# Optimization experiments

Measured on AMD Instinct MI355X. Metric: run time of the kernel, lower is better.

The kernel has to match this reference:

```python
import jax, jax.numpy as jnp
import numpy as np

B = 8; H = 128; W = 128; C = 256
NH = 16; HD = 16          # head_dim hard-coded to 16 in source
WS = 8; SS = 4            # window size / shift size
HID = 1024                # mlp hidden = 4 * C
SCALE = HD ** (-0.5)


def _rel_pos_index(ws):
    # same construction as torch buffer relative_position_index
    coords = np.stack(np.meshgrid(np.arange(ws), np.arange(ws), indexing='ij')).reshape(2, -1)
    rel = (coords[:, :, None] - coords[:, None, :]).transpose(1, 2, 0).copy()
    rel[..., 0] += ws - 1
    rel[..., 1] += ws - 1
    rel[..., 0] *= 2 * ws - 1
    return rel.sum(-1)  # (N, N) ints


def _attn_mask(h, w, ws, ss):
    # shifted-window mask, matches calculate_mask()
    img = np.zeros((h, w))
    sl = (slice(0, -ws), slice(-ws, -ss), slice(-ss, None))
    c = 0
    for hs in sl:
        for wsl in sl:
            img[hs, wsl] = c
            c += 1
    mw = img.reshape(h // ws, ws, w // ws, ws).transpose(0, 2, 1, 3).reshape(-1, ws * ws)
    d = mw[:, None, :] - mw[:, :, None]  # (nW, N, N)
    return np.where(d == 0, 0.0, -100.0).astype(np.float32)


def _ln(x, g, b, eps=1e-5):
    m = x.mean(-1, keepdims=True)
    v = ((x - m) ** 2).mean(-1, keepdims=True)
    return (x - m) * jax.lax.rsqrt(v + eps) * g + b


def setup_inputs() -> dict:
    key = jax.random.key(0)
    ks = jax.random.split(key, 12)
    inner = NH * HD
    std = 0.02
    return {
        'x': jax.random.normal(ks[0], (B, H * W, C), jnp.float32),
        'ln1_g': jnp.ones((C,), jnp.float32),
        'ln1_b': jnp.zeros((C,), jnp.float32),
        'q_w': jax.random.normal(ks[1], (C, inner), jnp.float32) * std,
        'q_b': jnp.zeros((inner,), jnp.float32),
        'k_w': jax.random.normal(ks[2], (C, inner), jnp.float32) * std,
        'k_b': jnp.zeros((inner,), jnp.float32),
        'v_w': jax.random.normal(ks[3], (C, inner), jnp.float32) * std,
        'v_b': jnp.zeros((inner,), jnp.float32),
        'rpb': jax.random.normal(ks[4], ((2 * WS - 1) * (2 * WS - 1), NH), jnp.float32) * std,
        'proj_w': jax.random.normal(ks[5], (inner, C), jnp.float32) * std,
        'proj_b': jnp.zeros((C,), jnp.float32),
        'ln2_g': jnp.ones((C,), jnp.float32),
        'ln2_b': jnp.zeros((C,), jnp.float32),
        'fc1_w': jax.random.normal(ks[6], (C, HID), jnp.float32) * std,
        'fc1_b': jnp.zeros((HID,), jnp.float32),
        'fc2_w': jax.random.normal(ks[7], (HID, C), jnp.float32) * std,
        'fc2_b': jnp.zeros((C,), jnp.float32),
        'H_in': 128,
        'W_in': 128,
    }


def reference(x, ln1_g, ln1_b, q_w, q_b, k_w, k_b, v_w, v_b, rpb,
              proj_w, proj_b, ln2_g, ln2_b, fc1_w, fc1_b, fc2_w, fc2_b,
              H_in, W_in):
    N = WS * WS
    nW = (H // WS) * (W // WS)
    idx = _rel_pos_index(WS)                       # static int (N, N)
    mask = jnp.asarray(_attn_mask(H, W, WS, SS))   # (nW, N, N)

    shortcut = x
    h = _ln(x, ln1_g, ln1_b).reshape(B, H, W, C)
    h = jnp.roll(h, (-SS, -SS), axis=(1, 2))
    # window partition -> (B*nW, N, C)
    h = h.reshape(B, H // WS, WS, W // WS, WS, C).transpose(0, 1, 3, 2, 4, 5)
    h = h.reshape(B * nW, N, C)

    q = (h @ q_w + q_b).reshape(-1, N, NH, HD).transpose(0, 2, 1, 3) * SCALE
    k = (h @ k_w + k_b).reshape(-1, N, NH, HD).transpose(0, 2, 1, 3)
    v = (h @ v_w + v_b).reshape(-1, N, NH, HD).transpose(0, 2, 1, 3)

    attn = jnp.einsum('bhnd,bhmd->bhnm', q, k)     # (B*nW, NH, N, N)
    bias = rpb[idx.reshape(-1)].reshape(N, N, NH).transpose(2, 0, 1)
    attn = attn + bias[None]
    attn = attn.reshape(B, nW, NH, N, N) + mask[None, :, None]
    attn = jax.nn.softmax(attn.reshape(B * nW, NH, N, N), axis=-1)

    o = jnp.einsum('bhnm,bhmd->bhnd', attn, v)
    o = o.transpose(0, 2, 1, 3).reshape(B * nW, N, NH * HD)
    o = o @ proj_w + proj_b

    # window reverse + roll back
    o = o.reshape(B, H // WS, W // WS, WS, WS, C).transpose(0, 1, 3, 2, 4, 5)
    o = o.reshape(B, H, W, C)
    o = jnp.roll(o, (SS, SS), axis=(1, 2)).reshape(B, H * W, C)

    x = shortcut + o
    h2 = _ln(x, ln2_g, ln2_b)
    h2 = jax.nn.gelu(h2 @ fc1_w + fc1_b, approximate=False)
    return x + (h2 @ fc2_w + fc2_b)
```

## Files before the change

kernel.cpp:

```cpp
#include <hip/hip_runtime.h>
#include <hip/hip_bf16.h>
#include <stdint.h>


#define SLOT ((size_t)64 << 20)

typedef __attribute__((ext_vector_type(8))) short bf16x8;
typedef __attribute__((ext_vector_type(4))) float f32x4;

union FU { float f; unsigned u; };

__device__ inline float bflo(unsigned p) { FU x; x.u = p << 16; return x.f; }
__device__ inline float bfhi(unsigned p) { FU x; x.u = p & 0xffff0000u; return x.f; }
__device__ inline unsigned short f2bf(float f) {
  FU x; x.f = f;
  unsigned r = x.u + 0x7fff + ((x.u >> 16) & 1);
  return (unsigned short)(r >> 16);
}
__device__ inline unsigned packbf2(float a, float b) {
  FU x, y; x.f = a; y.f = b;
  unsigned ra = (x.u + 0x7fff + ((x.u >> 16) & 1)) >> 16;
  unsigned rb = (y.u + 0x7fff + ((y.u >> 16) & 1)) & 0xffff0000u;
  return ra | rb;
}

__device__ inline float fast_gelu(float v) {
  return v / (1.0f + __expf(-1.702f * v));
}

__device__ inline void gload16(const void* g, void* l) {
  __builtin_amdgcn_global_load_lds(
      (const __attribute__((address_space(1))) unsigned int*)g,
      (__attribute__((address_space(3))) unsigned int*)l, 16, 0, 0);
}


__global__ __launch_bounds__(256) void build_qkvw(
    const float* __restrict__ qw, const float* __restrict__ kw, const float* __restrict__ vw,
    const float* __restrict__ qb, const float* __restrict__ kb, const float* __restrict__ vb,
    unsigned short* __restrict__ wt, float* __restrict__ bias) {
  int i = blockIdx.x * 256 + threadIdx.x;
  if (i < 768 * 256) {
    int n = i >> 8, c = i & 255;
    const float* w = (n < 256) ? qw : (n < 512 ? kw : vw);
    const float sc = (n < 256) ? 0.25f : 1.0f;
    int nn = n & 255;
    wt[i] = f2bf(sc * w[c * 256 + nn]);
  }
  if (i < 768) {
    bias[i] = (i < 256) ? 0.25f * qb[i] : (i < 512 ? kb[i - 256] : vb[i - 512]);
  }
}

__global__ __launch_bounds__(256) void wconv_t(
    const float* __restrict__ src, unsigned short* __restrict__ dst, int R, int C) {
  int i = blockIdx.x * 256 + threadIdx.x;
  if (i >= R * C) return;
  int n = i / R, c = i - n * R;
  dst[i] = f2bf(src[(size_t)c * C + n]);
}

__global__ __launch_bounds__(256) void ln1_roll_win(
    const float* __restrict__ x, const float* __restrict__ g, const float* __restrict__ b,
    unsigned short* __restrict__ hwin) {
  const int tok = blockIdx.x * 4 + (threadIdx.x >> 6);
  const int l = threadIdx.x & 63;
  const int n = tok & 63, wi = (tok >> 6) & 255, bb = tok >> 14;
  const int wh = wi >> 4, ww = wi & 15, r = n >> 3, c = n & 7;
  const int hs = (wh * 8 + r + 4) & 127;
  const int wsx = (ww * 8 + c + 4) & 127;
  const float* xr = x + ((size_t)bb * 16384 + hs * 128 + wsx) * 256;
  float4 v = *(const float4*)(xr + l * 4);
  float s = v.x + v.y + v.z + v.w;
#pragma unroll
  for (int off = 32; off; off >>= 1) s += __shfl_xor(s, off);
  const float mean = s * (1.f / 256.f);
  const float d0 = v.x - mean, d1 = v.y - mean, d2 = v.z - mean, d3 = v.w - mean;
  float vv = d0 * d0 + d1 * d1 + d2 * d2 + d3 * d3;
#pragma unroll
  for (int off = 32; off; off >>= 1) vv += __shfl_xor(vv, off);
  const float rs = rsqrtf(vv * (1.f / 256.f) + 1e-5f);
  float4 gg = *(const float4*)(g + l * 4);
  float4 bv = *(const float4*)(b + l * 4);
  uint2 outv;
  outv.x = packbf2(d0 * rs * gg.x + bv.x, d1 * rs * gg.y + bv.y);
  outv.y = packbf2(d2 * rs * gg.z + bv.z, d3 * rs * gg.w + bv.w);
  *(uint2*)(hwin + (size_t)tok * 256 + l * 4) = outv;
}

template <int EPI, int K, int N, int NBX>
__global__ __launch_bounds__(256) void gemm128(
    const unsigned short* __restrict__ A, const unsigned short* __restrict__ Bt,
    const float* __restrict__ bias, unsigned short* __restrict__ Cb,
    float* __restrict__ Cf) {
  __shared__ __align__(16) unsigned short smem[2][2][128 * 64];
  const int nwg = gridDim.x;
  const int q = nwg >> 3;
  const int swz = (blockIdx.x & 7) * q + (blockIdx.x >> 3);
  const int m0 = (swz / NBX) * 128;
  const int n0 = (swz % NBX) * 128;

  const int t = threadIdx.x, w = t >> 6, l = t & 63;
  const int lg = l >> 4, lm = l & 15;
  const int wr = w >> 1, wc = w & 1;

  const int srow = w * 32 + (l >> 3);
  const int scol = ((l & 7) ^ (l >> 3)) * 8;
  const unsigned short* Ap = A + (size_t)(m0 + srow) * K + scol;
  const unsigned short* Bp = Bt + (size_t)(n0 + srow) * K + scol;

  const int cb = n0 + wc * 64 + lm;
  f32x4 acc[4][4];
#pragma unroll
  for (int n = 0; n < 4; ++n) {
    const float bv = bias[cb + n * 16];
#pragma unroll
    for (int m = 0; m < 4; ++m) acc[m][n] = (f32x4){bv, bv, bv, bv};
  }

  constexpr int NT = K >> 6;
  const int cx = lg ^ (lm & 7);

#pragma unroll
  for (int i = 0; i < 4; ++i) {
    gload16(Ap + (size_t)(i * 8) * K, &smem[0][0][(w * 32 + i * 8) * 64]);
    gload16(Bp + (size_t)(i * 8) * K, &smem[0][1][(w * 32 + i * 8) * 64]);
  }
  __syncthreads();

#pragma unroll
  for (int kt = 0; kt < NT; ++kt) {
    const int cur = kt & 1;
    if (kt + 1 < NT) {
      const int ko = (kt + 1) << 6;
#pragma unroll
      for (int i = 0; i < 4; ++i) {
        gload16(Ap + (size_t)(i * 8) * K + ko, &smem[cur ^ 1][0][(w * 32 + i * 8) * 64]);
        gload16(Bp + (size_t)(i * 8) * K + ko, &smem[cur ^ 1][1][(w * 32 + i * 8) * 64]);
      }
    }
#pragma unroll
    for (int kk = 0; kk < 64; kk += 32) {
      const int ch = (cx ^ (kk >> 3)) * 8;
      bf16x8 af[4], bfr[4];
#pragma unroll
      for (int m = 0; m < 4; ++m)
        af[m] = *(const bf16x8*)&smem[cur][0][(wr * 64 + m * 16 + lm) * 64 + ch];
#pragma unroll
      for (int n = 0; n < 4; ++n)
        bfr[n] = *(const bf16x8*)&smem[cur][1][(wc * 64 + n * 16 + lm) * 64 + ch];
#pragma unroll
      for (int m = 0; m < 4; ++m)
#pragma unroll
        for (int n = 0; n < 4; ++n)
          acc[m][n] = __builtin_amdgcn_mfma_f32_16x16x32_bf16(af[m], bfr[n], acc[m][n], 0, 0, 0);
    }
    if (kt + 1 < NT) __syncthreads();
  }

  __syncthreads();
  float* Lp = (float*)smem;
#pragma unroll
  for (int m = 0; m < 4; ++m) {
#pragma unroll
    for (int n = 0; n < 4; ++n) {
      const int col = wc * 64 + n * 16 + lm;
#pragma unroll
      for (int r = 0; r < 4; ++r) {
        const int row = wr * 64 + m * 16 + lg * 4 + r;
        Lp[row * 128 + (col ^ (lg << 4))] = acc[m][n][r];
      }
    }
  }
  __syncthreads();
  const int rr0 = w * 32 + (l >> 5);
  const int cg = (l & 31) * 4;
#pragma unroll
  for (int p = 0; p < 16; ++p) {
    const int row = rr0 + p * 2;
    const int sc = cg ^ (((row >> 2) & 3) << 4);
    float4 v = *(const float4*)&Lp[row * 128 + sc];
    if (EPI == 2) {
      v.x = fast_gelu(v.x); v.y = fast_gelu(v.y);
      v.z = fast_gelu(v.z); v.w = fast_gelu(v.w);
    }
    if (EPI == 3) {
      float4* op = (float4*)&Cf[(size_t)(m0 + row) * N + n0 + cg];
      float4 o = *op;
      o.x += v.x; o.y += v.y; o.z += v.z; o.w += v.w;
      *op = o;
    } else {
      uint2 pk;
      pk.x = packbf2(v.x, v.y);
      pk.y = packbf2(v.z, v.w);
      *(uint2*)&Cb[(size_t)(m0 + row) * N + n0 + cg] = pk;
    }
  }
}

__global__ __launch_bounds__(512, 2) void proj_ln2(
    const unsigned short* __restrict__ A, const unsigned short* __restrict__ Bt,
    const float* __restrict__ bias, const float* __restrict__ x,
    const float* __restrict__ g2, const float* __restrict__ b2,
    float* __restrict__ out, unsigned short* __restrict__ h2) {
  constexpr int K = 256;
  __shared__ __align__(16) unsigned short smem[2][2][256 * 64];
  const int nwg = gridDim.x;
  const int q = nwg >> 3;
  const int swz = (blockIdx.x & 7) * q + (blockIdx.x >> 3);
  const int m0 = swz * 256;

  const int t = threadIdx.x, w = t >> 6, l = t & 63;
  const int lg = l >> 4, lm = l & 15;
  const int wr = w >> 2, wn = w & 3;

  const int srow = w * 8 + (l >> 3);
  const int scol = ((l & 7) ^ (l >> 3)) * 8;
  const unsigned short* Ap = A + (size_t)(m0 + srow) * K + scol;
  const unsigned short* Bp = Bt + (size_t)srow * K + scol;

  f32x4 acc[8][4];
#pragma unroll
  for (int n = 0; n < 4; ++n) {
    const float bv = bias[wn * 64 + n * 16 + lm];
#pragma unroll
    for (int m = 0; m < 8; ++m) acc[m][n] = (f32x4){bv, bv, bv, bv};
  }

  const int cx = lg ^ (lm & 7);

#pragma unroll
  for (int i = 0; i < 4; ++i) {
    gload16(Ap + (size_t)(i * 64) * K, &smem[0][0][(i * 64 + w * 8) * 64]);
    gload16(Bp + (size_t)(i * 64) * K, &smem[0][1][(i * 64 + w * 8) * 64]);
  }
  __syncthreads();

#pragma unroll
  for (int kt = 0; kt < 4; ++kt) {
    const int cur = kt & 1;
    if (kt + 1 < 4) {
      const int ko = (kt + 1) << 6;
#pragma unroll
      for (int i = 0; i < 4; ++i) {
        gload16(Ap + (size_t)(i * 64) * K + ko, &smem[cur ^ 1][0][(i * 64 + w * 8) * 64]);
        gload16(Bp + (size_t)(i * 64) * K + ko, &smem[cur ^ 1][1][(i * 64 + w * 8) * 64]);
      }
    }
#pragma unroll
    for (int kk = 0; kk < 64; kk += 32) {
      const int ch = (cx ^ (kk >> 3)) * 8;
      bf16x8 af[8], bfr[4];
#pragma unroll
      for (int m = 0; m < 8; ++m)
        af[m] = *(const bf16x8*)&smem[cur][0][(wr * 128 + m * 16 + lm) * 64 + ch];
#pragma unroll
      for (int n = 0; n < 4; ++n)
        bfr[n] = *(const bf16x8*)&smem[cur][1][(wn * 64 + n * 16 + lm) * 64 + ch];
#pragma unroll
      for (int m = 0; m < 8; ++m)
#pragma unroll
        for (int n = 0; n < 4; ++n)
          acc[m][n] = __builtin_amdgcn_mfma_f32_16x16x32_bf16(af[m], bfr[n], acc[m][n], 0, 0, 0);
    }
    if (kt + 1 < 4) __syncthreads();
  }

  float* Lf = (float*)smem;
  const float4 g4 = *(const float4*)(g2 + l * 4);
  const float4 bb4 = *(const float4*)(b2 + l * 4);
#pragma unroll
  for (int h = 0; h < 2; ++h) {
    __syncthreads();
    if (wr == h) {
#pragma unroll
      for (int m = 0; m < 8; ++m)
#pragma unroll
        for (int n = 0; n < 4; ++n) {
          const int col = wn * 64 + n * 16 + lm;
#pragma unroll
          for (int r = 0; r < 4; ++r) {
            const int rowl = m * 16 + lg * 4 + r;
            Lf[rowl * 256 + (col ^ (lg << 4))] = acc[m][n][r];
          }
        }
    }
    __syncthreads();
#pragma unroll
    for (int it = 0; it < 16; ++it) {
      const int rowl = it * 8 + w;
      const int sc = (l * 4) ^ (((rowl >> 2) & 3) << 4);
      float4 v = *(const float4*)&Lf[rowl * 256 + sc];
      const int src = m0 + h * 128 + rowl;
      const int bb = src >> 14, wi = (src >> 6) & 255, n = src & 63;
      const int hy = ((wi >> 4) * 8 + (n >> 3) + 4) & 127;
      const int wx = ((wi & 15) * 8 + (n & 7) + 4) & 127;
      const size_t dst = ((size_t)(bb << 14) + hy * 128 + wx) * 256;
      float4 xv = *(const float4*)(x + dst + l * 4);
      const float y0 = xv.x + v.x, y1 = xv.y + v.y;
      const float y2 = xv.z + v.z, y3 = xv.w + v.w;
      *(float4*)(out + dst + l * 4) = make_float4(y0, y1, y2, y3);
      float s = y0 + y1 + y2 + y3;
#pragma unroll
      for (int off = 32; off; off >>= 1) s += __shfl_xor(s, off);
      const float mean = s * (1.f / 256.f);
      const float d0 = y0 - mean, d1 = y1 - mean, d2 = y2 - mean, d3 = y3 - mean;
      float vv = d0 * d0 + d1 * d1 + d2 * d2 + d3 * d3;
#pragma unroll
      for (int off = 32; off; off >>= 1) vv += __shfl_xor(vv, off);
      const float rs = rsqrtf(vv * (1.f / 256.f) + 1e-5f);
      uint2 outv;
      outv.x = packbf2(d0 * rs * g4.x + bb4.x, d1 * rs * g4.y + bb4.y);
      outv.y = packbf2(d2 * rs * g4.z + bb4.z, d3 * rs * g4.w + bb4.w);
      *(uint2*)(h2 + dst + l * 4) = outv;
    }
  }
}

__global__ __launch_bounds__(256) void attn_mfma(
    const unsigned short* __restrict__ qkv, const float* __restrict__ rpb,
    unsigned short* __restrict__ o) {
  __shared__ float rps[16][226];
  __shared__ __align__(16) unsigned short Pl[4][64][72];
  const int win = blockIdx.x;
  const int wh = (win >> 4) & 15, ww = win & 15;
  const int t = threadIdx.x, wv = t >> 6, l = t & 63;
  const int lg = l >> 4, lm = l & 15;
  const unsigned short* base = qkv + (size_t)win * 64 * 768;

  for (int i = t; i < 3600; i += 256) rps[i & 15][i >> 4] = rpb[i];
  __syncthreads();

  const bool eH = (wh == 15), eW = (ww == 15);
  const bool edge = eH || eW;

  int qv[4], liq[4];
#pragma unroll
  for (int nt = 0; nt < 4; ++nt) {
    const int qn = nt * 16 + lm, ri = qn >> 3, ci = qn & 7;
    qv[nt] = ri * 15 + ci;
    liq[nt] = (eH ? (ri < 4 ? 1 : 2) : 0) * 3 + (eW ? (ci < 4 ? 1 : 2) : 0);
  }
  int kv[4][4], ljk[4][4];
#pragma unroll
  for (int mt = 0; mt < 4; ++mt)
#pragma unroll
    for (int r = 0; r < 4; ++r) {
      const int kn = mt * 16 + 4 * lg + r, rj = kn >> 3, cj = kn & 7;
      kv[mt][r] = rj * 15 + cj;
      ljk[mt][r] = (eH ? (rj < 4 ? 1 : 2) : 0) * 3 + (eW ? (cj < 4 ? 1 : 2) : 0);
    }

  const bf16x8 zf = {0, 0, 0, 0, 0, 0, 0, 0};

#pragma unroll 1
  for (int hi = 0; hi < 4; ++hi) {
    const int h = wv * 4 + hi;
    bf16x8 kf[4], qf[4];
#pragma unroll
    for (int i = 0; i < 4; ++i) {
      kf[i] = (lg < 2)
          ? *(const bf16x8*)(base + (size_t)(i * 16 + lm) * 768 + 256 + h * 16 + lg * 8)
          : zf;
      qf[i] = (lg < 2)
          ? *(const bf16x8*)(base + (size_t)(i * 16 + lm) * 768 + h * 16 + lg * 8)
          : zf;
    }
    f32x4 acc[4][4];
#pragma unroll
    for (int mt = 0; mt < 4; ++mt)
#pragma unroll
      for (int nt = 0; nt < 4; ++nt)
        acc[mt][nt] = (f32x4){0.f, 0.f, 0.f, 0.f};
#pragma unroll
    for (int mt = 0; mt < 4; ++mt)
#pragma unroll
      for (int nt = 0; nt < 4; ++nt)
        acc[mt][nt] = __builtin_amdgcn_mfma_f32_16x16x32_bf16(kf[mt], qf[nt], acc[mt][nt], 0, 0, 0);

#pragma unroll
    for (int nt = 0; nt < 4; ++nt) {
      float mx = -1e30f;
#pragma unroll
      for (int mt = 0; mt < 4; ++mt)
#pragma unroll
        for (int r = 0; r < 4; ++r) {
          float s = acc[mt][nt][r] + rps[h][qv[nt] - kv[mt][r] + 112];
          if (edge) s += (liq[nt] == ljk[mt][r]) ? 0.f : -100.f;
          acc[mt][nt][r] = s;
          mx = fmaxf(mx, s);
        }
      mx = fmaxf(mx, __shfl_xor(mx, 16));
      mx = fmaxf(mx, __shfl_xor(mx, 32));
      float sum = 0.f;
#pragma unroll
      for (int mt = 0; mt < 4; ++mt)
#pragma unroll
        for (int r = 0; r < 4; ++r) {
          const float p = __expf(acc[mt][nt][r] - mx);
          acc[mt][nt][r] = p;
          sum += p;
        }
      sum += __shfl_xor(sum, 16);
      sum += __shfl_xor(sum, 32);
      const float inv = 1.f / sum;
      const int qn = nt * 16 + lm;
#pragma unroll
      for (int mt = 0; mt < 4; ++mt) {
        uint2 pk;
        pk.x = packbf2(acc[mt][nt][0] * inv, acc[mt][nt][1] * inv);
        pk.y = packbf2(acc[mt][nt][2] * inv, acc[mt][nt][3] * inv);
        *(uint2*)&Pl[wv][qn][mt * 16 + 4 * lg] = pk;
      }
    }

    f32x4 oacc[4];
#pragma unroll
    for (int mt = 0; mt < 4; ++mt) oacc[mt] = (f32x4){0.f, 0.f, 0.f, 0.f};
#pragma unroll
    for (int kk = 0; kk < 2; ++kk) {
      bf16x8 vf;
#pragma unroll
      for (int j = 0; j < 8; ++j)
        vf[j] = (short)base[(size_t)(kk * 32 + lg * 8 + j) * 768 + 512 + h * 16 + lm];
#pragma unroll
      for (int mt = 0; mt < 4; ++mt) {
        bf16x8 pf = *(const bf16x8*)&Pl[wv][mt * 16 + lm][kk * 32 + lg * 8];
        oacc[mt] = __builtin_amdgcn_mfma_f32_16x16x32_bf16(pf, vf, oacc[mt], 0, 0, 0);
      }
    }
#pragma unroll
    for (int mt = 0; mt < 4; ++mt)
#pragma unroll
      for (int r = 0; r < 4; ++r)
        o[((size_t)win * 64 + mt * 16 + 4 * lg + r) * 256 + h * 16 + lm] = f2bf(oacc[mt][r]);
  }
}


extern "C" void kernel_launch(void* const* d_in, const int* in_sizes, int n_in,
                              void* d_out, int out_size, void* d_ws, size_t ws_size,
                              hipStream_t stream) {
  const float* x = (const float*)d_in[0];
  const float* ln1g = (const float*)d_in[1];
  const float* ln1b = (const float*)d_in[2];
  const float* qw = (const float*)d_in[3];
  const float* qb = (const float*)d_in[4];
  const float* kw = (const float*)d_in[5];
  const float* kb = (const float*)d_in[6];
  const float* vw = (const float*)d_in[7];
  const float* vb = (const float*)d_in[8];
  const float* rpb = (const float*)d_in[9];
  const float* pw = (const float*)d_in[10];
  const float* pb = (const float*)d_in[11];
  const float* ln2g = (const float*)d_in[12];
  const float* ln2b = (const float*)d_in[13];
  const float* f1w = (const float*)d_in[14];
  const float* f1b = (const float*)d_in[15];
  const float* f2w = (const float*)d_in[16];
  const float* f2b = (const float*)d_in[17];
  float* out = (float*)d_out;

  char* wsb = (char*)d_ws;
  unsigned short* hwin = (unsigned short*)(wsb);
  unsigned short* qkv = (unsigned short*)(wsb + SLOT);
  unsigned short* ovec = (unsigned short*)(wsb + 4 * SLOT);
  unsigned short* g1 = qkv;
  unsigned short* wqkvt = (unsigned short*)(wsb + 5 * SLOT);
  unsigned short* projt = wqkvt + 768 * 256;
  unsigned short* fc1t = projt + 256 * 256;
  unsigned short* fc2t = fc1t + 1024 * 256;
  float* bqkv = (float*)(fc2t + 256 * 1024);

  build_qkvw<<<768, 256, 0, stream>>>(qw, kw, vw, qb, kb, vb, wqkvt, bqkv);
  wconv_t<<<256, 256, 0, stream>>>(pw, projt, 256, 256);
  wconv_t<<<1024, 256, 0, stream>>>(f1w, fc1t, 256, 1024);
  wconv_t<<<1024, 256, 0, stream>>>(f2w, fc2t, 1024, 256);

  ln1_roll_win<<<32768, 256, 0, stream>>>(x, ln1g, ln1b, hwin);
  gemm128<0, 256, 768, 6><<<6 * 1024, 256, 0, stream>>>(hwin, wqkvt, bqkv, qkv, nullptr);
  attn_mfma<<<2048, 256, 0, stream>>>(qkv, rpb, ovec);
  proj_ln2<<<512, 512, 0, stream>>>(ovec, projt, pb, x, ln2g, ln2b, out, hwin);
  gemm128<2, 256, 1024, 8><<<8 * 1024, 256, 0, stream>>>(hwin, fc1t, f1b, g1, nullptr);
  gemm128<3, 1024, 256, 2><<<2 * 1024, 256, 0, stream>>>(g1, fc2t, f2b, nullptr, out);
}
```

Measured before the change: 685.7 us.

## Use 256x128 GEMM tiles with 512 threads and triple-buffered async loads

Replaces the 128x128, 256-thread, double-buffered GEMM with a 256x128 tile computed by 8 waves. The B tile is shared across twice as many rows, and a 3-stage LDS ring with explicit vmcnt waits and raw s_barrier keeps two stages of loads in flight. This is meant to hide global-load latency better and halve B-operand traffic per output. In exchange the kernel uses more LDS (about 144 KB) and runs one workgroup per CU, and the hand-counted vmcnt values must match the number of loads issued.

```diff
diff --git a/kernel.cpp b/kernel.cpp
--- a/kernel.cpp
+++ b/kernel.cpp
@@ -88,104 +88,113 @@
   *(uint2*)(hwin + (size_t)tok * 256 + l * 4) = outv;
 }
 
+#define STAGE(b, kt)                                                         \
+  {                                                                          \
+    const int ko_ = (kt) * 64;                                               \
+    _Pragma("unroll") for (int i_ = 0; i_ < 4; ++i_)                         \
+        gload16(Ap + (size_t)(i_ * 8) * K + ko_,                             \
+                &smem[b][(w * 32 + i_ * 8) * 64]);                           \
+    _Pragma("unroll") for (int i_ = 0; i_ < 2; ++i_)                         \
+        gload16(Bp + (size_t)(i_ * 8) * K + ko_,                             \
+                &smem[b][(256 + w * 16 + i_ * 8) * 64]);                     \
+  }
+
 template <int EPI, int K, int N, int NBX>
-__global__ __launch_bounds__(256) void gemm128(
+__global__ __launch_bounds__(512, 1) void gemmp(
     const unsigned short* __restrict__ A, const unsigned short* __restrict__ Bt,
     const float* __restrict__ bias, unsigned short* __restrict__ Cb,
     float* __restrict__ Cf) {
-  __shared__ __align__(16) unsigned short smem[2][2][128 * 64];
+  constexpr int NT = K >> 6;
+  __shared__ __align__(16) unsigned short smem[3][384 * 64];
   const int nwg = gridDim.x;
   const int q = nwg >> 3;
   const int swz = (blockIdx.x & 7) * q + (blockIdx.x >> 3);
-  const int m0 = (swz / NBX) * 128;
+  const int m0 = (swz / NBX) * 256;
   const int n0 = (swz % NBX) * 128;
 
   const int t = threadIdx.x, w = t >> 6, l = t & 63;
   const int lg = l >> 4, lm = l & 15;
   const int wr = w >> 1, wc = w & 1;
 
-  const int srow = w * 32 + (l >> 3);
   const int scol = ((l & 7) ^ (l >> 3)) * 8;
-  const unsigned short* Ap = A + (size_t)(m0 + srow) * K + scol;
-  const unsigned short* Bp = Bt + (size_t)(n0 + srow) * K + scol;
-
-  const int cb = n0 + wc * 64 + lm;
+  const unsigned short* Ap = A + (size_t)(m0 + w * 32 + (l >> 3)) * K + scol;
+  const unsigned short* Bp = Bt + (size_t)(n0 + w * 16 + (l >> 3)) * K + scol;
+
   f32x4 acc[4][4];
 #pragma unroll
   for (int n = 0; n < 4; ++n) {
-    const float bv = bias[cb + n * 16];
+    const float bv = bias[n0 + wc * 64 + n * 16 + lm];
 #pragma unroll
     for (int m = 0; m < 4; ++m) acc[m][n] = (f32x4){bv, bv, bv, bv};
   }
 
-  constexpr int NT = K >> 6;
   const int cx = lg ^ (lm & 7);
 
-#pragma unroll
-  for (int i = 0; i < 4; ++i) {
-    gload16(Ap + (size_t)(i * 8) * K, &smem[0][0][(w * 32 + i * 8) * 64]);
-    gload16(Bp + (size_t)(i * 8) * K, &smem[0][1][(w * 32 + i * 8) * 64]);
-  }
-  __syncthreads();
+  STAGE(0, 0);
+  STAGE(1, 1);
+  STAGE(2, 2);
+  asm volatile("s_waitcnt vmcnt(12)" ::: "memory");
+  __builtin_amdgcn_s_barrier();
 
 #pragma unroll
   for (int kt = 0; kt < NT; ++kt) {
-    const int cur = kt & 1;
-    if (kt + 1 < NT) {
-      const int ko = (kt + 1) << 6;
-#pragma unroll
-      for (int i = 0; i < 4; ++i) {
-        gload16(Ap + (size_t)(i * 8) * K + ko, &smem[cur ^ 1][0][(w * 32 + i * 8) * 64]);
-        gload16(Bp + (size_t)(i * 8) * K + ko, &smem[cur ^ 1][1][(w * 32 + i * 8) * 64]);
-      }
-    }
+    const int cur = kt % 3;
 #pragma unroll
     for (int kk = 0; kk < 64; kk += 32) {
       const int ch = (cx ^ (kk >> 3)) * 8;
       bf16x8 af[4], bfr[4];
 #pragma unroll
       for (int m = 0; m < 4; ++m)
-        af[m] = *(const bf16x8*)&smem[cur][0][(wr * 64 + m * 16 + lm) * 64 + ch];
+        af[m] = *(const bf16x8*)&smem[cur][(wr * 64 + m * 16 + lm) * 64 + ch];
 #pragma unroll
       for (int n = 0; n < 4; ++n)
-        bfr[n] = *(const bf16x8*)&smem[cur][1][(wc * 64 + n * 16 + lm) * 64 + ch];
+        bfr[n] = *(const bf16x8*)&smem[cur][(256 + wc * 64 + n * 16 + lm) * 64 + ch];
 #pragma unroll
       for (int m = 0; m < 4; ++m)
 #pragma unroll
         for (int n = 0; n < 4; ++n)
           acc[m][n] = __builtin_amdgcn_mfma_f32_16x16x32_bf16(af[m], bfr[n], acc[m][n], 0, 0, 0);
     }
-    if (kt + 1 < NT) __syncthreads();
-  }
-
-  __syncthreads();
-  float* Lp = (float*)smem;
-#pragma unroll
-  for (int m = 0; m < 4; ++m) {
+    __builtin_amdgcn_s_barrier();
+    if (kt + 3 < NT) STAGE(cur, kt + 3);
+    if (kt + 1 < NT) {
+      if (kt + 3 < NT) {
+        asm volatile("s_waitcnt vmcnt(12)" ::: "memory");
+      } else if (kt + 2 < NT) {
+        asm volatile("s_waitcnt vmcnt(6)" ::: "memory");
+      } else {
+        asm volatile("s_waitcnt vmcnt(0)" ::: "memory");
+      }
+      __builtin_amdgcn_s_barrier();
+    }
+  }
+
+  float* Lf = (float*)smem;
+#pragma unroll
+  for (int m = 0; m < 4; ++m)
 #pragma unroll
     for (int n = 0; n < 4; ++n) {
       const int col = wc * 64 + n * 16 + lm;
 #pragma unroll
       for (int r = 0; r < 4; ++r) {
         const int row = wr * 64 + m * 16 + lg * 4 + r;
-        Lp[row * 128 + (col ^ (lg << 4))] = acc[m][n][r];
+        Lf[row * 128 + (col ^ (lg << 4))] = acc[m][n][r];
       }
     }
-  }
   __syncthreads();
-  const int rr0 = w * 32 + (l >> 5);
-  const int cg = (l & 31) * 4;
 #pragma unroll
   for (int p = 0; p < 16; ++p) {
-    const int row = rr0 + p * 2;
-    const int sc = cg ^ (((row >> 2) & 3) << 4);
-    float4 v = *(const float4*)&Lp[row * 128 + sc];
+    const int fidx = p * 512 + t;
+    const int row = fidx >> 5;
+    const int c4 = (fidx & 31) * 4;
+    const int sc = c4 ^ (((row >> 2) & 3) << 4);
+    float4 v = *(const float4*)&Lf[row * 128 + sc];
     if (EPI == 2) {
       v.x = fast_gelu(v.x); v.y = fast_gelu(v.y);
       v.z = fast_gelu(v.z); v.w = fast_gelu(v.w);
     }
     if (EPI == 3) {
-      float4* op = (float4*)&Cf[(size_t)(m0 + row) * N + n0 + cg];
+      float4* op = (float4*)&Cf[(size_t)(m0 + row) * N + n0 + c4];
       float4 o = *op;
       o.x += v.x; o.y += v.y; o.z += v.z; o.w += v.w;
       *op = o;
@@ -193,7 +202,7 @@
       uint2 pk;
       pk.x = packbf2(v.x, v.y);
       pk.y = packbf2(v.z, v.w);
-      *(uint2*)&Cb[(size_t)(m0 + row) * N + n0 + cg] = pk;
+      *(uint2*)&Cb[(size_t)(m0 + row) * N + n0 + c4] = pk;
     }
   }
 }
@@ -478,9 +487,9 @@
   wconv_t<<<1024, 256, 0, stream>>>(f2w, fc2t, 1024, 256);
 
   ln1_roll_win<<<32768, 256, 0, stream>>>(x, ln1g, ln1b, hwin);
-  gemm128<0, 256, 768, 6><<<6 * 1024, 256, 0, stream>>>(hwin, wqkvt, bqkv, qkv, nullptr);
+  gemmp<0, 256, 768, 6><<<512 * 6, 512, 0, stream>>>(hwin, wqkvt, bqkv, qkv, nullptr);
   attn_mfma<<<2048, 256, 0, stream>>>(qkv, rpb, ovec);
   proj_ln2<<<512, 512, 0, stream>>>(ovec, projt, pb, x, ln2g, ln2b, out, hwin);
-  gemm128<2, 256, 1024, 8><<<8 * 1024, 256, 0, stream>>>(hwin, fc1t, f1b, g1, nullptr);
-  gemm128<3, 1024, 256, 2><<<2 * 1024, 256, 0, stream>>>(g1, fc2t, f2b, nullptr, out);
-}
+  gemmp<2, 256, 1024, 8><<<512 * 8, 512, 0, stream>>>(hwin, fc1t, f1b, g1, nullptr);
+  gemmp<3, 1024, 256, 2><<<512 * 2, 512, 0, stream>>>(g1, fc2t, f2b, nullptr, out);
+}
```

Result: slower. 727.3 us (+6.1%).

## Fuse fc1+GELU+fc2 MLP into one kernel keeping hidden activations in LDS

Applied to the files above, without the earlier changes.

Replaces the two separate MLP GEMM launches with one fused kernel. Each 64-token block computes fc1 in 256-wide hidden chunks, applies bias and GELU, stores the bf16 result in shared memory, and accumulates fc2 directly, then adds into the residual output. This removes the global write and re-read of the 1024-wide hidden tensor. In exchange, weights are read straight from global memory without LDS staging and the per-block tile is smaller, which risks lower MFMA efficiency and more weight traffic.

```diff
diff --git a/kernel.cpp b/kernel.cpp
--- a/kernel.cpp
+++ b/kernel.cpp
@@ -195,6 +195,125 @@
       pk.y = packbf2(v.z, v.w);
       *(uint2*)&Cb[(size_t)(m0 + row) * N + n0 + cg] = pk;
     }
+  }
+}
+
+__global__ __launch_bounds__(256, 2) void fused_mlp(
+    const unsigned short* __restrict__ h2, const unsigned short* __restrict__ w1t,
+    const float* __restrict__ b1, const unsigned short* __restrict__ w2t,
+    const float* __restrict__ b2, float* __restrict__ out) {
+  __shared__ __align__(16) unsigned short smem[2 * 64 * 256];
+  unsigned short* As = smem;
+  unsigned short* Hs = smem + 64 * 256;
+  const int nwg = gridDim.x;
+  const int q = nwg >> 3;
+  const int swz = (blockIdx.x & 7) * q + (blockIdx.x >> 3);
+  const int m0 = swz * 64;
+
+  const int t = threadIdx.x, w = t >> 6, l = t & 63;
+  const int lg = l >> 4, lm = l & 15;
+
+#pragma unroll
+  for (int i = 0; i < 8; ++i) {
+    const int row = w * 16 + i * 2 + (l >> 5);
+    const int sc = (l & 31) ^ (row & 7);
+    gload16(h2 + (size_t)(m0 + row) * 256 + sc * 8, &As[(w * 16 + i * 2) * 256]);
+  }
+
+  f32x4 oacc[4][4];
+#pragma unroll
+  for (int n = 0; n < 4; ++n) {
+    const float bv = b2[w * 64 + n * 16 + lm];
+#pragma unroll
+    for (int m = 0; m < 4; ++m) oacc[m][n] = (f32x4){bv, bv, bv, bv};
+  }
+  __syncthreads();
+
+  for (int hc = 0; hc < 4; ++hc) {
+    if (hc) __syncthreads();
+    f32x4 a1[4][4];
+#pragma unroll
+    for (int mh = 0; mh < 4; ++mh)
+#pragma unroll
+      for (int nt = 0; nt < 4; ++nt) a1[mh][nt] = (f32x4){0.f, 0.f, 0.f, 0.f};
+#pragma unroll
+    for (int kk = 0; kk < 8; ++kk) {
+      bf16x8 aw[4], bt[4];
+#pragma unroll
+      for (int mh = 0; mh < 4; ++mh)
+        aw[mh] = *(const bf16x8*)(w1t +
+                 (size_t)(hc * 256 + w * 64 + mh * 16 + lm) * 256 + kk * 32 + lg * 8);
+#pragma unroll
+      for (int nt = 0; nt < 4; ++nt) {
+        const int c2 = (kk * 4 + lg) ^ (lm & 7);
+        bt[nt] = *(const bf16x8*)&As[(nt * 16 + lm) * 256 + c2 * 8];
+      }
+#pragma unroll
+      for (int mh = 0; mh < 4; ++mh)
+#pragma unroll
+        for (int nt = 0; nt < 4; ++nt)
+          a1[mh][nt] = __builtin_amdgcn_mfma_f32_16x16x32_bf16(aw[mh], bt[nt], a1[mh][nt], 0, 0, 0);
+    }
+#pragma unroll
+    for (int mh = 0; mh < 4; ++mh) {
+      const float4 b1f = *(const float4*)&b1[hc * 256 + w * 64 + mh * 16 + lg * 4];
+#pragma unroll
+      for (int nt = 0; nt < 4; ++nt) {
+        const int tok = nt * 16 + lm;
+        const int cp = (w * 16 + mh * 4 + lg) ^ ((lm & 7) << 1);
+        uint2 pk;
+        pk.x = packbf2(fast_gelu(a1[mh][nt][0] + b1f.x), fast_gelu(a1[mh][nt][1] + b1f.y));
+        pk.y = packbf2(fast_gelu(a1[mh][nt][2] + b1f.z), fast_gelu(a1[mh][nt][3] + b1f.w));
+        *(uint2*)((char*)Hs + tok * 512 + cp * 8) = pk;
+      }
+    }
+    __syncthreads();
+#pragma unroll
+    for (int kk = 0; kk < 8; ++kk) {
+      bf16x8 ah[4], bw2[4];
+#pragma unroll
+      for (int mt = 0; mt < 4; ++mt) {
+        const int tok = mt * 16 + lm;
+        const int cp = (kk * 8 + lg * 2) ^ ((lm & 7) << 1);
+        ah[mt] = *(const bf16x8*)((const char*)Hs + tok * 512 + cp * 8);
+      }
+#pragma unroll
+      for (int n = 0; n < 4; ++n)
+        bw2[n] = *(const bf16x8*)(w2t +
+                 (size_t)(w * 64 + n * 16 + lm) * 1024 + hc * 256 + kk * 32 + lg * 8);
+#pragma unroll
+      for (int mt = 0; mt < 4; ++mt)
+#pragma unroll
+        for (int n = 0; n < 4; ++n)
+          oacc[mt][n] = __builtin_amdgcn_mfma_f32_16x16x32_bf16(ah[mt], bw2[n], oacc[mt][n], 0, 0, 0);
+    }
+  }
+
+  __syncthreads();
+  float* Lt = (float*)smem;
+#pragma unroll
+  for (int m = 0; m < 4; ++m)
+#pragma unroll
+    for (int n = 0; n < 4; ++n) {
+      const int col = w * 64 + n * 16 + lm;
+#pragma unroll
+      for (int r = 0; r < 4; ++r) {
+        const int row = m * 16 + lg * 4 + r;
+        Lt[row * 256 + (col ^ (lg << 4))] = oacc[m][n][r];
+      }
+    }
+  __syncthreads();
+#pragma unroll
+  for (int p = 0; p < 16; ++p) {
+    const int fidx = p * 256 + t;
+    const int row = fidx >> 6;
+    const int c4 = (fidx & 63) * 4;
+    const int sc = c4 ^ (((row >> 2) & 3) << 4);
+    float4 v = *(const float4*)&Lt[row * 256 + sc];
+    float4* op = (float4*)&out[(size_t)(m0 + row) * 256 + c4];
+    float4 o = *op;
+    o.x += v.x; o.y += v.y; o.z += v.z; o.w += v.w;
+    *op = o;
   }
 }
 
@@ -465,7 +584,6 @@
   unsigned short* hwin = (unsigned short*)(wsb);
   unsigned short* qkv = (unsigned short*)(wsb + SLOT);
   unsigned short* ovec = (unsigned short*)(wsb + 4 * SLOT);
-  unsigned short* g1 = qkv;
   unsigned short* wqkvt = (unsigned short*)(wsb + 5 * SLOT);
   unsigned short* projt = wqkvt + 768 * 256;
   unsigned short* fc1t = projt + 256 * 256;
@@ -481,6 +599,5 @@
   gemm128<0, 256, 768, 6><<<6 * 1024, 256, 0, stream>>>(hwin, wqkvt, bqkv, qkv, nullptr);
   attn_mfma<<<2048, 256, 0, stream>>>(qkv, rpb, ovec);
   proj_ln2<<<512, 512, 0, stream>>>(ovec, projt, pb, x, ln2g, ln2b, out, hwin);
-  gemm128<2, 256, 1024, 8><<<8 * 1024, 256, 0, stream>>>(hwin, fc1t, f1b, g1, nullptr);
-  gemm128<3, 1024, 256, 2><<<2 * 1024, 256, 0, stream>>>(g1, fc2t, f2b, nullptr, out);
-}
+  fused_mlp<<<2048, 256, 0, stream>>>(hwin, fc1t, f1b, fc2t, f2b, out);
+}
```

Measured after the change: 696.1 us. About the same (+1.5%).
